# Kernel tuning notes

Hardware: AMD Instinct MI355X
Metric: run time of the kernel (lower is better)

The kernel has to match this reference:

```python
import jax, jax.numpy as jnp
import numpy as np

B, DIM, RANK, H, W = 16, 64, 32, 128, 128
E, K, BINS, FREQ_DIM, KS = 4, 2, 8, 64, 7
NOISE_STD = 1.0 / E


def dwconv(x, w, b, pad):
    # depthwise conv, NCHW, weight [C,1,kh,kw]
    y = jax.lax.conv_general_dilated(x, w, (1, 1), [(pad, pad), (pad, pad)],
        dimension_numbers=('NCHW', 'OIHW', 'NCHW'), feature_group_count=x.shape[1])
    return y + b[None, :, None, None]


def avgpool3(x):
    # AvgPool2d(3, stride=1, padding=1), count_include_pad=True -> sum/9
    s = jax.lax.reduce_window(x, 0.0, jax.lax.add, (1, 1, 3, 3), (1, 1, 1, 1),
        [(0, 0), (0, 0), (1, 1), (1, 1)])
    return s / 9.0


def freq_filter(x, gain, decay, cmax):
    # HighFreqGlobal / LowFreqGlobal: rfft2 -> scale magnitude by radial filter -> irfft2
    Bh, C, Hh, Wh = x.shape
    xf = jnp.fft.rfft2(x, norm='ortho')
    mag, ph = jnp.abs(xf), jnp.angle(xf)
    fy = jnp.fft.fftfreq(Hh).astype(x.dtype)[:, None]
    fx = jnp.fft.rfftfreq(Wh).astype(x.dtype)[None, :]
    fg = jnp.sqrt(fy ** 2 + fx ** 2)
    filt = jnp.clip((1.0 - jnp.exp(-gain * fg)) * jnp.exp(-decay * fg), 0.0, cmax)
    return jnp.fft.irfft2((mag * filt) * jnp.exp(1j * ph), s=(Hh, Wh), norm='ortho')


def freq_energy(x):
    # RoutingFunction.get_frequency_energy: radial energy histogram over BINS bins
    Bh, C, Hh, Wh = x.shape
    mag = jnp.abs(jnp.fft.fft2(x, norm='forward'))
    gy = jnp.arange(-Hh // 2, Hh // 2, dtype=jnp.float32)[:, None]
    gx = jnp.arange(-Wh // 2, Wh // 2, dtype=jnp.float32)[None, :]
    dist = jnp.sqrt(gy ** 2 + gx ** 2)
    edges = jnp.linspace(0.0, dist.max(), BINS + 1)
    masks = ((dist[None] >= edges[:-1, None, None]) & (dist[None] < edges[1:, None, None])).astype(mag.dtype)
    return jnp.einsum('bchw,khw->bk', mag, masks) / C  # sum over HW then mean over C


def setup_inputs():
    key = jax.random.key(0)
    ks = jax.random.split(key, 16)
    p = lambda k, shp, s=0.02: jax.random.normal(k, shp, jnp.float32) * s
    return {
        'x': jax.random.normal(ks[0], (B, DIM, H, W), jnp.float32),
        'noise': jax.random.normal(ks[1], (B, E), jnp.float32),
        'gate_w': p(ks[2], (E, DIM)),
        'fg_w1': p(ks[3], (FREQ_DIM, BINS)),
        'fg_b1': jnp.zeros((FREQ_DIM,), jnp.float32),
        'fg_w2': p(ks[4], (E, FREQ_DIM)),
        'proj0': p(ks[5], (E, RANK, DIM)),
        'proj1': p(ks[6], (E, RANK, DIM)),
        'proj2': p(ks[7], (E, DIM, RANK)),
        'hg_gain': jnp.float32(2.0),
        'hg_decay': jnp.float32(0.5),
        'hf_w1': p(ks[8], (RANK, 1, 3, 3), 0.1),
        'hf_b1': jnp.zeros((RANK,), jnp.float32),
        'hf_w2': p(ks[9], (RANK, 1, 3, 3), 0.1),
        'hf_b2': jnp.zeros((RANK,), jnp.float32),
        'lg_gain': jnp.float32(1.0),
        'lg_decay': jnp.float32(1.0),
        'lf_w': p(ks[10], (RANK, 1, KS, KS), 0.1),
        'lf_b': jnp.zeros((RANK,), jnp.float32),
    }


def reference(x, noise, gate_w, fg_w1, fg_b1, fg_w2, proj0, proj1, proj2,
              hg_gain, hg_decay, hf_w1, hf_b1, hf_w2, hf_b2,
              lg_gain, lg_decay, lf_w, lf_b):
    Bh = x.shape[0]
    # routing: image gate (GAP + linear) + frequency gate (MLP on radial energy)
    img_logits = jnp.mean(x, axis=(2, 3)) @ gate_w.T
    femb = freq_energy(x)
    hidden = jax.nn.relu(femb @ fg_w1.T + fg_b1)
    logits = img_logits + hidden @ fg_w2.T
    scores = jax.nn.softmax(logits + noise * NOISE_STD, axis=-1)
    vals, idx = jax.lax.top_k(scores, K)
    gates = jnp.zeros_like(scores).at[jnp.arange(Bh)[:, None], idx].set(vals)

    def expert(e, body):
        # ModExpert.process: low-rank proj -> body * silu(gate proj of shared=x) -> up proj + shortcut
        h = jnp.einsum('bchw,rc->brhw', x, proj0[e])
        g = jax.nn.silu(jnp.einsum('bchw,rc->brhw', x, proj1[e]))
        h = body(h) * g
        return jnp.einsum('brhw,cr->bchw', h, proj2[e]) + x

    gelu = lambda z: jax.nn.gelu(z, approximate=False)
    bodies = [
        lambda z: freq_filter(z, hg_gain, hg_decay, 3.0),                          # HighFreqGlobal
        lambda z: dwconv(gelu(dwconv(z, hf_w1, hf_b1, 1)), hf_w2, hf_b2, 1),       # HighFreqLocal
        lambda z: freq_filter(z, lg_gain, lg_decay, 1.0),                          # LowFreqGlobal
        lambda z: avgpool3(gelu(dwconv(z, lf_w, lf_b, KS // 2))),                  # LowFreqLocal
    ]
    # dispatch/combine expressed densely: gates are exactly zero for non-selected experts,
    # so weighted sum == SparseDispatcher.combine
    out = jnp.zeros_like(x)
    for e, body in enumerate(bodies):
        out = out + gates[:, e][:, None, None, None] * expert(e, body)
    return out
```

## Files before the change

### kernel.cpp

```cpp
#include <hip/hip_runtime.h>
#include <math.h>


namespace {

struct cpx { float x, y; };
struct TwB {
  cpx t0;
  cpx ws[6];
  float sg[6];
};

using bf16x8 = __attribute__((ext_vector_type(8))) short;
using f32x4  = __attribute__((ext_vector_type(4))) float;

__device__ __forceinline__ short f2bf(float f){
  unsigned u = __float_as_uint(f);
  u += 0x7FFF + ((u >> 16) & 1);
  return (short)(u >> 16);
}

__device__ __forceinline__ cpx cmul(cpx a, cpx b){ return {a.x*b.x - a.y*b.y, a.x*b.y + a.y*b.x}; }

__device__ __forceinline__ void init_twb(TwB &T, int lane, const float2* __restrict__ tw128){
  float2 v0 = tw128[lane];
  T.t0 = {v0.x, v0.y};
  int m = 32;
  #pragma unroll
  for (int s = 0; s < 6; s++){
    bool up = (lane & m) != 0;
    float2 wv = tw128[(lane & (m-1)) * (64/m)];
    T.ws[s] = up ? cpx{wv.x, wv.y} : cpx{1.0f, 0.0f};
    T.sg[s] = up ? -1.0f : 1.0f;
    m >>= 1;
  }
}

__device__ __forceinline__ int br6(int l){ return (int)(__brev((unsigned)l) >> 26); }
__device__ __forceinline__ int pos7(int j){ return ((j & 1) << 6) | (j >> 1); }

__device__ __forceinline__ void fft128(cpx &a, cpx &b, int lane, const TwB &T){
  cpx u{a.x + b.x, a.y + b.y};
  cpx v{a.x - b.x, a.y - b.y};
  v = cmul(v, T.t0);
  a = u; b = v;
  int m = 32;
  #pragma unroll
  for (int s = 0; s < 6; s++){
    float pax = __shfl_xor(a.x, m);
    float pay = __shfl_xor(a.y, m);
    float pbx = __shfl_xor(b.x, m);
    float pby = __shfl_xor(b.y, m);
    float sg = T.sg[s];
    cpx w = T.ws[s];
    cpx ta{fmaf(sg, a.x, pax), fmaf(sg, a.y, pay)};
    cpx tb{fmaf(sg, b.x, pbx), fmaf(sg, b.y, pby)};
    a = cmul(ta, w);
    b = cmul(tb, w);
    m >>= 1;
  }
}

__device__ __forceinline__ float gelu_exact(float v){
  return 0.5f * v * (1.0f + erff(v * 0.70710678118654752f));
}

__device__ __forceinline__ float silu(float v){
  return v / (1.0f + expf(-v));
}


__global__ __launch_bounds__(256) void k_transW(const float* __restrict__ proj0, float* __restrict__ p0t,
                                                float2* __restrict__ tw128){
  int t = threadIdx.x;
  if (t < 128){
    float s, c;
    sincosf(-6.283185307179586f * (float)t * (1.0f/128.0f), &s, &c);
    tw128[t] = make_float2(c, s);
  }
  for (int idx = t; idx < 2048; idx += 256){
    int r = idx >> 6, c = idx & 63;
    p0t[0*2048 + c*32 + r] = proj0[0*2048 + idx];
    p0t[1*2048 + c*32 + r] = proj0[2*2048 + idx];
  }
}

__global__ __launch_bounds__(512) void k_fft2fwd(const float* __restrict__ x, float2* __restrict__ X,
                                                 float* __restrict__ part_w, float* __restrict__ xmean,
                                                 const float2* __restrict__ tw128){
  __shared__ float2 z[8192];
  int bc = blockIdx.x; int t = threadIdx.x;
  int lane = t & 63, wv = t >> 6;
  TwB T; init_twb(T, lane, tw128);
  const float* img = x + (size_t)bc * 16384;
  int rb = br6(lane);

  #pragma unroll 4
  for (int k = 0; k < 8; k++){
    int p = wv*8 + k;
    int h0 = 2*p, h1 = 2*p + 1;
    cpx a{img[h0*128 + lane],      img[h1*128 + lane]};
    cpx b{img[h0*128 + lane + 64], img[h1*128 + lane + 64]};
    fft128(a, b, lane, T);
    int ia = (p << 7) | (rb ^ p);
    z[ia]      = make_float2(a.x, a.y);
    z[ia | 64] = make_float2(b.x, b.y);
  }
  __syncthreads();

  float rax[8], ray[8], rbx[8], rby[8];
  #pragma unroll
  for (int k = 0; k < 8; k++){
    int jj = wv*8 + k;
    int p  = lane >> 1, s = lane & 1;
    int p2 = 32 + p;
    cpx a, b;
    if (jj == 0){
      float2 z0  = z[(p << 7)  | (0  ^ p)];
      float2 z64 = z[(p << 7)  | (32 ^ p)];
      float2 w0  = z[(p2 << 7) | (0  ^ p2)];
      float2 w64 = z[(p2 << 7) | (32 ^ p2)];
      a = { s ? z0.y : z0.x, s ? z64.y : z64.x };
      b = { s ? w0.y : w0.x, s ? w64.y : w64.x };
    } else {
      int jm = 128 - jj;
      int pj = pos7(jj), pm = pos7(jm);
      float2 z1 = z[(p << 7) | (pj ^ p)],  z2 = z[(p << 7) | (pm ^ p)];
      if (s == 0) a = { 0.5f*(z1.x + z2.x), 0.5f*(z1.y - z2.y) };
      else        a = { 0.5f*(z1.y + z2.y), 0.5f*(z2.x - z1.x) };
      float2 w1 = z[(p2 << 7) | (pj ^ p2)], w2 = z[(p2 << 7) | (pm ^ p2)];
      if (s == 0) b = { 0.5f*(w1.x + w2.x), 0.5f*(w1.y - w2.y) };
      else        b = { 0.5f*(w1.y + w2.y), 0.5f*(w2.x - w1.x) };
    }
    fft128(a, b, lane, T);
    rax[k] = a.x; ray[k] = a.y; rbx[k] = b.x; rby[k] = b.y;
  }
  __syncthreads();
  #pragma unroll
  for (int k = 0; k < 8; k++){
    int jj = wv*8 + k;
    int ia = (jj << 7) | (rb ^ jj);
    z[ia]      = make_float2(rax[k], ray[k]);
    z[ia | 64] = make_float2(rbx[k], rby[k]);
  }
  __syncthreads();

  if (t == 0) xmean[bc] = z[0].x * (1.0f/16384.0f);

  float edges[9];
  float step = sqrtf(8192.0f) * 0.125f;
  #pragma unroll
  for (int k = 0; k <= 8; k++) edges[k] = step * (float)k;
  float acc[8] = {0,0,0,0,0,0,0,0};
  for (int idx = t; idx < 64*128; idx += 512){
    int j = idx >> 7, i = idx & 127;
    if (j == 0){
      float2 c0 = z[pos7(i)];
      int in_ = (128 - i) & 127;
      float2 d0v = z[pos7(in_)];
      float x0r = 0.5f*(c0.x + d0v.x), x0i = 0.5f*(c0.y - d0v.y);
      float x6r = 0.5f*(c0.y + d0v.y), x6i = 0.5f*(d0v.x - c0.x);
      float m0 = sqrtf(x0r*x0r + x0i*x0i) * (1.0f/16384.0f);
      float m6 = sqrtf(x6r*x6r + x6i*x6i) * (1.0f/16384.0f);
      float dyv = (float)(i - 64);
      float d0 = sqrtf(dyv*dyv + 4096.0f);
      float d6 = fabsf(dyv);
      #pragma unroll
      for (int k = 0; k < 8; k++){
        if (d0 >= edges[k] && d0 < edges[k+1]) acc[k] += m0;
        if (d6 >= edges[k] && d6 < edges[k+1]) acc[k] += m6;
      }
    } else {
      float2 zv = z[(j << 7) | (pos7(i) ^ j)];
      float mag = sqrtf(zv.x*zv.x + zv.y*zv.y) * (2.0f/16384.0f);
      float dy = (float)(i - 64), dx = (float)(j - 64);
      float d = sqrtf(dy*dy + dx*dx);
      #pragma unroll
      for (int k = 0; k < 8; k++)
        if (d >= edges[k] && d < edges[k+1]) acc[k] += mag;
    }
  }
  #pragma unroll
  for (int k = 0; k < 8; k++){
    float v = acc[k];
    for (int off = 32; off > 0; off >>= 1) v += __shfl_xor(v, off);
    if (lane == 0) part_w[(bc*8 + wv)*8 + k] = v;
  }

  float2* Xo = X + (size_t)bc * (65*128);
  for (int idx = t; idx < 65*128; idx += 512){
    int j = idx >> 7, i = idx & 127;
    float2 v;
    if (j == 0){
      float2 c0 = z[pos7(i)];
      int in_ = (128 - i) & 127;
      float2 d0v = z[pos7(in_)];
      v = make_float2(0.5f*(c0.x + d0v.x), 0.5f*(c0.y - d0v.y));
    } else if (j == 64){
      float2 c0 = z[pos7(i)];
      int in_ = (128 - i) & 127;
      float2 d0v = z[pos7(in_)];
      v = make_float2(0.5f*(c0.y + d0v.y), 0.5f*(d0v.x - c0.x));
    } else {
      v = z[(j << 7) | (pos7(i) ^ j)];
    }
    Xo[idx] = v;
  }
}

__global__ __launch_bounds__(128) void k_routing(const float* __restrict__ xmean, const float* __restrict__ part_w,
    const float* __restrict__ noise, const float* __restrict__ gate_w,
    const float* __restrict__ fg_w1, const float* __restrict__ fg_b1, const float* __restrict__ fg_w2,
    int* __restrict__ slot_e, int* __restrict__ slot_of, float* __restrict__ slot_g){
  __shared__ float femb[16][8];
  __shared__ float hid[16][64];
  __shared__ float lgt[16][4];
  int t = threadIdx.x;
  {
    int b = t >> 3, k = t & 7;
    float s = 0.f;
    for (int c = 0; c < 64; c++)
      for (int w = 0; w < 8; w++)
        s += part_w[((b*64 + c)*8 + w)*8 + k];
    femb[b][k] = s * (1.0f/64.0f);
  }
  __syncthreads();
  for (int idx = t; idx < 16*64; idx += 128){
    int b = idx >> 6, f = idx & 63;
    float s = fg_b1[f];
    for (int k = 0; k < 8; k++) s += femb[b][k] * fg_w1[f*8 + k];
    hid[b][f] = fmaxf(s, 0.f);
  }
  __syncthreads();
  if (t < 64){
    int b = t >> 2, e = t & 3;
    float s = 0.f;
    for (int c = 0; c < 64; c++) s += xmean[b*64 + c] * gate_w[e*64 + c];
    for (int f = 0; f < 64; f++) s += hid[b][f] * fg_w2[e*64 + f];
    lgt[b][e] = s + noise[b*4 + e] * 0.25f;
  }
  __syncthreads();
  if (t < 16){
    int b = t;
    float m = fmaxf(fmaxf(lgt[b][0], lgt[b][1]), fmaxf(lgt[b][2], lgt[b][3]));
    float p[4]; float sum = 0.f;
    for (int e = 0; e < 4; e++){ p[e] = expf(lgt[b][e] - m); sum += p[e]; }
    for (int e = 0; e < 4; e++) p[e] /= sum;
    int i1 = 0;
    for (int e = 1; e < 4; e++) if (p[e] > p[i1]) i1 = e;
    int i2 = -1;
    for (int e = 0; e < 4; e++){ if (e == i1) continue; if (i2 < 0 || p[e] > p[i2]) i2 = e; }
    slot_e[b*2 + 0] = i1;
    slot_e[b*2 + 1] = i2;
    slot_g[b*2 + 0] = p[i1];
    slot_g[b*2 + 1] = p[i2];
    for (int e = 0; e < 4; e++) slot_of[b*4 + e] = (e == i1) ? 0 : ((e == i2) ? 1 : -1);
  }
}

__global__ __launch_bounds__(256) void k_projfreq(const float2* __restrict__ X, const float* __restrict__ p0t,
    float2* __restrict__ Y, const int* __restrict__ slot_e,
    const float* __restrict__ hg_gain, const float* __restrict__ hg_decay,
    const float* __restrict__ lg_gain, const float* __restrict__ lg_decay){
  int b = blockIdx.z;
  int e0 = __builtin_amdgcn_readfirstlane(slot_e[b*2 + 0]);
  int e1 = __builtin_amdgcn_readfirstlane(slot_e[b*2 + 1]);
  bool f0 = (e0 == 0) || (e0 == 2);
  bool f1 = (e1 == 0) || (e1 == 2);
  if (!f0 && !f1) return;
  int j = blockIdx.y;
  int i0 = blockIdx.x * 64;
  int t = threadIdx.x;
  int lane = t & 63;
  int w = __builtin_amdgcn_readfirstlane(t >> 6);
  __shared__ float2 sx[64][64];
  for (int idx = t; idx < 4096; idx += 256){
    int c = idx >> 6, ii = idx & 63;
    sx[c][ii] = X[(((size_t)(b*64 + c))*65 + j)*128 + i0 + ii];
  }
  __syncthreads();
  int i = i0 + lane;
  const float* W0 = p0t + ((f0 ? (e0 >> 1) : (e1 >> 1)) * 2048) + w*8;
  const float* W1 = p0t + ((f1 ? (e1 >> 1) : (e0 >> 1)) * 2048) + w*8;
  float a0x[8] = {0,0,0,0,0,0,0,0}, a0y[8] = {0,0,0,0,0,0,0,0};
  float a1x[8] = {0,0,0,0,0,0,0,0}, a1y[8] = {0,0,0,0,0,0,0,0};
  for (int c = 0; c < 64; c++){
    float2 xv = sx[c][lane];
    const float* wc0 = W0 + c*32;
    const float* wc1 = W1 + c*32;
    #pragma unroll
    for (int k = 0; k < 8; k++){
      float w0v = wc0[k];
      a0x[k] += w0v * xv.x; a0y[k] += w0v * xv.y;
      float w1v = wc1[k];
      a1x[k] += w1v * xv.x; a1y[k] += w1v * xv.y;
    }
  }
  float fy = (float)(i < 64 ? i : i - 128) * (1.0f/128.0f);
  float fx = (float)j * (1.0f/128.0f);
  float fg = sqrtf(fy*fy + fx*fx);
  if (f0){
    float gain, decay, cmax;
    if (e0 == 0){ gain = *hg_gain; decay = *hg_decay; cmax = 3.0f; }
    else        { gain = *lg_gain; decay = *lg_decay; cmax = 1.0f; }
    float filt = (1.0f - expf(-gain*fg)) * expf(-decay*fg);
    filt = fminf(fmaxf(filt, 0.0f), cmax) * (1.0f/16384.0f);
    int bs = b*2 + 0;
    #pragma unroll
    for (int k = 0; k < 8; k++){
      int r = w*8 + k;
      Y[((size_t)(bs*32 + r))*8320 + j*128 + i] = make_float2(a0x[k]*filt, a0y[k]*filt);
    }
  }
  if (f1){
    float gain, decay, cmax;
    if (e1 == 0){ gain = *hg_gain; decay = *hg_decay; cmax = 3.0f; }
    else        { gain = *lg_gain; decay = *lg_decay; cmax = 1.0f; }
    float filt = (1.0f - expf(-gain*fg)) * expf(-decay*fg);
    filt = fminf(fmaxf(filt, 0.0f), cmax) * (1.0f/16384.0f);
    int bs = b*2 + 1;
    #pragma unroll
    for (int k = 0; k < 8; k++){
      int r = w*8 + k;
      Y[((size_t)(bs*32 + r))*8320 + j*128 + i] = make_float2(a1x[k]*filt, a1y[k]*filt);
    }
  }
}

__global__ __launch_bounds__(512) void k_ifft2(float2* __restrict__ Y, const int* __restrict__ slot_e,
                                               const float2* __restrict__ tw128){
  int blk = blockIdx.x;
  int bs = blk >> 5, r = blk & 31;
  int es = slot_e[bs];
  if (es == 1 || es == 3) return;
  __shared__ float2 z[8192];
  int t = threadIdx.x; int lane = t & 63, wv = t >> 6;
  TwB T; init_twb(T, lane, tw128);
  int rb = br6(lane);
  float2* Yb = Y + (size_t)(bs*32 + r) * 8320;

  for (int idx = t; idx < 8192; idx += 512){
    int j = idx >> 7, i = idx & 127;
    if (j == 0){
      float2 y0 = Yb[i];
      float2 y6 = Yb[8192 + i];
      z[pos7(i)] = make_float2(y0.x - y6.y, y0.y + y6.x);
    } else {
      z[(j << 7) | (pos7(i) ^ j)] = Yb[idx];
    }
  }
  __syncthreads();

  #pragma unroll
  for (int k = 0; k < 8; k++){
    int jj = wv*8 + k;
    float2 z0 = z[(jj << 7) | (pos7(lane) ^ jj)];
    float2 z1 = z[(jj << 7) | ((pos7(lane) + 32) ^ jj)];
    cpx a{z0.x, -z0.y}, b{z1.x, -z1.y};
    fft128(a, b, lane, T);
    int ia = (jj << 7) | (rb ^ jj);
    z[ia]      = make_float2(a.x, -a.y);
    z[ia | 64] = make_float2(b.x, -b.y);
  }
  __syncthreads();

  float* body = (float*)Yb;
  #pragma unroll 2
  for (int k = 0; k < 8; k++){
    int p = wv*8 + k;
    int h = 2*p, h1 = 2*p + 1;
    int ph = pos7(h), ph1 = pos7(h1);
    cpx a, b;
    if (lane == 0){
      float2 c0 = z[ph], c1 = z[ph1];
      a = { c0.x, c1.x };
      b = { c0.y, c1.y };
    } else {
      float2 yh = z[(lane << 7) | (ph ^ lane)];
      float2 y1 = z[(lane << 7) | (ph1 ^ lane)];
      a = { yh.x - y1.y, yh.y + y1.x };
      int lm = 64 - lane;
      float2 zh  = z[(lm << 7) | (ph ^ lm)];
      float2 z1_ = z[(lm << 7) | (ph1 ^ lm)];
      b = { zh.x + z1_.y, z1_.x - zh.y };
    }
    a.y = -a.y; b.y = -b.y;
    fft128(a, b, lane, T);
    int n0 = 2*rb;
    body[h*128 + n0]      = a.x;
    body[h1*128 + n0]     = -a.y;
    body[h*128 + n0 + 1]  = b.x;
    body[h1*128 + n0 + 1] = -b.y;
  }
}

__global__ __launch_bounds__(256) void k_projA(const float* __restrict__ x, const float* __restrict__ proj0,
    const int* __restrict__ slot_e, float* __restrict__ A){
  int b = blockIdx.y;
  int e0 = __builtin_amdgcn_readfirstlane(slot_e[b*2 + 0]);
  int e1 = __builtin_amdgcn_readfirstlane(slot_e[b*2 + 1]);
  bool c0 = (e0 == 1) || (e0 == 3);
  bool c1 = (e1 == 1) || (e1 == 3);
  if (!c0 && !c1) return;
  __shared__ unsigned short xs[128][72];
  int px0 = blockIdx.x * 128;
  int t = threadIdx.x;
  int w = t >> 6, lane = t & 63;
  int h = lane & 15, g = lane >> 4;
  const float* xb = x + (size_t)b*64*16384;

  for (int idx = t; idx < 2048; idx += 256){
    int c = idx >> 5, pq = idx & 31;
    float4 v = *(const float4*)&xb[(size_t)c*16384 + px0 + pq*4];
    xs[pq*4 + 0][c] = (unsigned short)f2bf(v.x);
    xs[pq*4 + 1][c] = (unsigned short)f2bf(v.y);
    xs[pq*4 + 2][c] = (unsigned short)f2bf(v.z);
    xs[pq*4 + 3][c] = (unsigned short)f2bf(v.w);
  }

  bf16x8 af[2][2][2];
  #pragma unroll
  for (int s = 0; s < 2; s++){
    bool cv = (s == 0) ? c0 : c1;
    if (!cv) continue;
    int e = (s == 0) ? e0 : e1;
    const float* P0 = proj0 + e*2048;
    #pragma unroll
    for (int mr = 0; mr < 2; mr++)
      #pragma unroll
      for (int k0 = 0; k0 < 2; k0++){
        const float* p = P0 + (mr*16 + h)*64 + k0*32 + g*8;
        bf16x8 v;
        #pragma unroll
        for (int j = 0; j < 8; j++) v[j] = f2bf(p[j]);
        af[s][mr][k0] = v;
      }
  }
  __syncthreads();

  int pxw = w*32;
  #pragma unroll
  for (int nt = 0; nt < 2; nt++){
    int pxl = pxw + nt*16;
    int px  = px0 + pxl;
    bf16x8 bx[2];
    #pragma unroll
    for (int k0 = 0; k0 < 2; k0++)
      bx[k0] = *(bf16x8*)&xs[pxl + h][k0*32 + g*8];
    #pragma unroll
    for (int s = 0; s < 2; s++){
      bool cv = (s == 0) ? c0 : c1;
      if (!cv) continue;
      float* Ab = A + (size_t)((b*2 + s)*32)*16384;
      #pragma unroll
      for (int mr = 0; mr < 2; mr++){
        f32x4 acc = {0.f, 0.f, 0.f, 0.f};
        acc = __builtin_amdgcn_mfma_f32_16x16x32_bf16(af[s][mr][0], bx[0], acc, 0, 0, 0);
        acc = __builtin_amdgcn_mfma_f32_16x16x32_bf16(af[s][mr][1], bx[1], acc, 0, 0, 0);
        #pragma unroll
        for (int reg = 0; reg < 4; reg++){
          int r = mr*16 + g*4 + reg;
          Ab[(size_t)r*16384 + px + h] = acc[reg];
        }
      }
    }
  }
}

__global__ __launch_bounds__(256) void k_conv3(const float* __restrict__ A, float* __restrict__ bodyY,
    const float* __restrict__ w1g, const float* __restrict__ b1g,
    const float* __restrict__ w2g, const float* __restrict__ b2g,
    const int* __restrict__ slot_of){
  int by = blockIdx.y; int b = by >> 5, r = by & 31;
  int slot = slot_of[b*4 + 1];
  if (slot < 0) return;
  int bs = b*2 + slot;
  int h0 = blockIdx.x * 16;
  int t = threadIdx.x;
  __shared__ float sin_[20*130];
  __shared__ float st[18*130];
  for (int i = t; i < 20*130; i += 256) sin_[i] = 0.f;
  for (int i = t; i < 18*130; i += 256) st[i] = 0.f;
  float w1[9], w2[9];
  #pragma unroll
  for (int k = 0; k < 9; k++){ w1[k] = w1g[r*9 + k]; w2[k] = w2g[r*9 + k]; }
  float b1 = b1g[r], b2 = b2g[r];
  __syncthreads();
  const float* ip = A + (size_t)(bs*32 + r)*16384;
  for (int idx = t; idx < 20*128; idx += 256){
    int li = idx >> 7, ww = idx & 127;
    int ih = h0 - 2 + li;
    if (ih >= 0 && ih < 128) sin_[li*130 + 1 + ww] = ip[ih*128 + ww];
  }
  __syncthreads();
  for (int idx = t; idx < 18*128; idx += 256){
    int li = idx >> 7, ww = idx & 127;
    int hs = h0 - 1 + li;
    if (hs >= 0 && hs < 128){
      float acc = b1;
      #pragma unroll
      for (int kh = 0; kh < 3; kh++)
        #pragma unroll
        for (int kw = 0; kw < 3; kw++)
          acc += w1[kh*3 + kw] * sin_[(li + kh)*130 + ww + kw];
      st[li*130 + 1 + ww] = gelu_exact(acc);
    }
  }
  __syncthreads();
  float* op = bodyY + (size_t)(bs*32 + r)*16640;
  for (int idx = t; idx < 16*128; idx += 256){
    int li = idx >> 7, ww = idx & 127;
    int ho = h0 + li;
    float acc = b2;
    #pragma unroll
    for (int kh = 0; kh < 3; kh++)
      #pragma unroll
      for (int kw = 0; kw < 3; kw++)
        acc += w2[kh*3 + kw] * st[(li + kh)*130 + ww + kw];
    op[ho*128 + ww] = acc;
  }
}

__global__ __launch_bounds__(256) void k_conv7(const float* __restrict__ A, float* __restrict__ bodyY,
    const float* __restrict__ wg, const float* __restrict__ bg,
    const int* __restrict__ slot_of){
  int by = blockIdx.y; int b = by >> 5, r = by & 31;
  int slot = slot_of[b*4 + 3];
  if (slot < 0) return;
  int bs = b*2 + slot;
  int h0 = blockIdx.x * 16;
  int t = threadIdx.x;
  __shared__ float sin_[24*134];
  __shared__ float st[18*134];
  __shared__ float wsh[49];
  for (int i = t; i < 24*134; i += 256) sin_[i] = 0.f;
  for (int i = t; i < 18*134; i += 256) st[i] = 0.f;
  if (t < 49) wsh[t] = wg[r*49 + t];
  float bias = bg[r];
  __syncthreads();
  const float* ip = A + (size_t)(bs*32 + r)*16384;
  for (int idx = t; idx < 24*128; idx += 256){
    int li = idx >> 7, ww = idx & 127;
    int ih = h0 - 4 + li;
    if (ih >= 0 && ih < 128) sin_[li*134 + 3 + ww] = ip[ih*128 + ww];
  }
  __syncthreads();
  for (int idx = t; idx < 18*128; idx += 256){
    int li = idx >> 7, ww = idx & 127;
    int hs = h0 - 1 + li;
    if (hs >= 0 && hs < 128){
      float acc = bias;
      #pragma unroll
      for (int kh = 0; kh < 7; kh++)
        #pragma unroll
        for (int kw = 0; kw < 7; kw++)
          acc += wsh[kh*7 + kw] * sin_[(li + kh)*134 + ww + kw];
      st[li*134 + 1 + ww] = gelu_exact(acc);
    }
  }
  __syncthreads();
  float* op = bodyY + (size_t)(bs*32 + r)*16640;
  for (int idx = t; idx < 16*128; idx += 256){
    int li = idx >> 7, ww = idx & 127;
    int ho = h0 + li;
    float acc = 0.f;
    #pragma unroll
    for (int kh = 0; kh < 3; kh++)
      #pragma unroll
      for (int kw = 0; kw < 3; kw++)
        acc += st[(li + kh)*134 + ww + kw];
    op[ho*128 + ww] = acc * (1.0f/9.0f);
  }
}

__global__ __launch_bounds__(256) void k_combine(const float* __restrict__ x, const float* __restrict__ bodyY,
    const float* __restrict__ proj1, const float* __restrict__ proj2,
    const int* __restrict__ slot_e, const float* __restrict__ slot_g,
    float* __restrict__ out){
  __shared__ __align__(16) unsigned char smem[57344];
  unsigned short (*xs)[72]            = (unsigned short(*)[72])(smem);
  unsigned short (*bs2)[128][36]      = (unsigned short(*)[128][36])(smem + 18432);
  unsigned short (*sblk)[4][2][16][40] = (unsigned short(*)[4][2][16][40])(smem + 36864);
  float* obuf = (float*)smem;

  int b = blockIdx.y;
  int px0 = blockIdx.x * 128;
  int t = threadIdx.x;
  int w = t >> 6, lane = t & 63;
  int h = lane & 15, g = lane >> 4;
  int ea = __builtin_amdgcn_readfirstlane(slot_e[b*2 + 0]);
  int eb = __builtin_amdgcn_readfirstlane(slot_e[b*2 + 1]);
  float ga = slot_g[b*2 + 0], gb = slot_g[b*2 + 1];
  float gs = ga + gb;

  const float* xb = x + (size_t)b*64*16384;
  float* ob = out + (size_t)b*64*16384;
  const float* Bd0 = bodyY + (size_t)(b*2 + 0)*32*16640;
  const float* Bd1 = bodyY + (size_t)(b*2 + 1)*32*16640;

  for (int idx = t; idx < 2048; idx += 256){
    int c = idx >> 5, pq = idx & 31;
    float4 v = *(const float4*)&xb[(size_t)c*16384 + px0 + pq*4];
    xs[pq*4 + 0][c] = (unsigned short)f2bf(v.x);
    xs[pq*4 + 1][c] = (unsigned short)f2bf(v.y);
    xs[pq*4 + 2][c] = (unsigned short)f2bf(v.z);
    xs[pq*4 + 3][c] = (unsigned short)f2bf(v.w);
  }
  for (int idx = t; idx < 2048; idx += 256){
    int s = idx >> 10, r = (idx >> 5) & 31, pq = idx & 31;
    const float* Bod = (s == 0) ? Bd0 : Bd1;
    float4 v = *(const float4*)&Bod[(size_t)r*16640 + px0 + pq*4];
    bs2[s][pq*4 + 0][r] = (unsigned short)f2bf(v.x);
    bs2[s][pq*4 + 1][r] = (unsigned short)f2bf(v.y);
    bs2[s][pq*4 + 2][r] = (unsigned short)f2bf(v.z);
    bs2[s][pq*4 + 3][r] = (unsigned short)f2bf(v.w);
  }

  bf16x8 a1[2][2][2];
  #pragma unroll
  for (int s = 0; s < 2; s++){
    const float* P1 = proj1 + (s == 0 ? ea : eb)*2048;
    #pragma unroll
    for (int mr = 0; mr < 2; mr++)
      #pragma unroll
      for (int k0 = 0; k0 < 2; k0++){
        const float* p = P1 + (mr*16 + h)*64 + k0*32 + g*8;
        bf16x8 v;
        #pragma unroll
        for (int j = 0; j < 8; j++) v[j] = f2bf(p[j]);
        a1[s][mr][k0] = v;
      }
  }
  bf16x8 a2[2][4];
  #pragma unroll
  for (int s = 0; s < 2; s++){
    const float* P2 = proj2 + (s == 0 ? ea : eb)*2048;
    #pragma unroll
    for (int mc = 0; mc < 4; mc++){
      const float* p = P2 + (mc*16 + h)*32 + g*8;
      bf16x8 v;
      #pragma unroll
      for (int j = 0; j < 8; j++) v[j] = f2bf(p[j]);
      a2[s][mc] = v;
    }
  }
  __syncthreads();

  int pxw = w*32;
  #pragma unroll
  for (int nt = 0; nt < 2; nt++){
    int pxl = pxw + nt*16;
    bf16x8 bx[2];
    #pragma unroll
    for (int k0 = 0; k0 < 2; k0++)
      bx[k0] = *(bf16x8*)&xs[pxl + h][k0*32 + g*8];
    f32x4 acc1[2][2];
    #pragma unroll
    for (int s = 0; s < 2; s++)
      #pragma unroll
      for (int mr = 0; mr < 2; mr++){
        f32x4 acc = {0.f, 0.f, 0.f, 0.f};
        acc = __builtin_amdgcn_mfma_f32_16x16x32_bf16(a1[s][mr][0], bx[0], acc, 0, 0, 0);
        acc = __builtin_amdgcn_mfma_f32_16x16x32_bf16(a1[s][mr][1], bx[1], acc, 0, 0, 0);
        acc1[s][mr] = acc;
      }
    #pragma unroll
    for (int s = 0; s < 2; s++){
      float gw = (s == 0) ? ga : gb;
      #pragma unroll
      for (int mr = 0; mr < 2; mr++){
        int r0 = mr*16 + g*4;
        unsigned short b4[4];
        *(uint2*)b4 = *(uint2*)&bs2[s][pxl + h][r0];
        unsigned pk0, pk1;
        {
          float bv0 = __uint_as_float(((unsigned)b4[0]) << 16);
          float bv1 = __uint_as_float(((unsigned)b4[1]) << 16);
          float bv2 = __uint_as_float(((unsigned)b4[2]) << 16);
          float bv3 = __uint_as_float(((unsigned)b4[3]) << 16);
          float s0 = gw * bv0 * silu(acc1[s][mr][0]);
          float s1 = gw * bv1 * silu(acc1[s][mr][1]);
          float s2 = gw * bv2 * silu(acc1[s][mr][2]);
          float s3 = gw * bv3 * silu(acc1[s][mr][3]);
          pk0 = (unsigned)(unsigned short)f2bf(s0) | ((unsigned)(unsigned short)f2bf(s1) << 16);
          pk1 = (unsigned)(unsigned short)f2bf(s2) | ((unsigned)(unsigned short)f2bf(s3) << 16);
        }
        uint2 pv; pv.x = pk0; pv.y = pk1;
        *(uint2*)&sblk[nt][w][s][h][r0] = pv;
      }
    }
  }
  __syncthreads();

  #pragma unroll
  for (int nt = 0; nt < 2; nt++){
    bf16x8 sb0 = *(bf16x8*)&sblk[nt][w][0][h][g*8];
    bf16x8 sb1 = *(bf16x8*)&sblk[nt][w][1][h][g*8];
    #pragma unroll
    for (int mc = 0; mc < 4; mc++){
      f32x4 acc = {0.f, 0.f, 0.f, 0.f};
      acc = __builtin_amdgcn_mfma_f32_16x16x32_bf16(a2[0][mc], sb0, acc, 0, 0, 0);
      acc = __builtin_amdgcn_mfma_f32_16x16x32_bf16(a2[1][mc], sb1, acc, 0, 0, 0);
      #pragma unroll
      for (int reg = 0; reg < 4; reg++){
        int c = mc*16 + g*4 + reg;
        obuf[(w*64 + c)*36 + nt*16 + h] = acc[reg];
      }
    }
  }
  int fq = lane & 7, cr = lane >> 3;
  const float* xw = xb + px0 + w*32;
  float* ow = ob + px0 + w*32;
  #pragma unroll
  for (int i = 0; i < 8; i++){
    int c = i*8 + cr;
    float4 v = *(float4*)&obuf[(w*64 + c)*36 + fq*4];
    float4 xv4 = *(const float4*)&xw[(size_t)c*16384 + fq*4];
    *(float4*)&ow[(size_t)c*16384 + fq*4] =
      make_float4(gs*xv4.x + v.x, gs*xv4.y + v.y, gs*xv4.z + v.z, gs*xv4.w + v.w);
  }
}

}

extern "C" void kernel_launch(void* const* d_in, const int* in_sizes, int n_in,
                              void* d_out, int out_size, void* d_ws, size_t ws_size,
                              hipStream_t stream) {
  (void)in_sizes; (void)n_in; (void)out_size; (void)ws_size;
  const float* x        = (const float*)d_in[0];
  const float* noise    = (const float*)d_in[1];
  const float* gate_w   = (const float*)d_in[2];
  const float* fg_w1    = (const float*)d_in[3];
  const float* fg_b1    = (const float*)d_in[4];
  const float* fg_w2    = (const float*)d_in[5];
  const float* proj0    = (const float*)d_in[6];
  const float* proj1    = (const float*)d_in[7];
  const float* proj2    = (const float*)d_in[8];
  const float* hg_gain  = (const float*)d_in[9];
  const float* hg_decay = (const float*)d_in[10];
  const float* hf_w1    = (const float*)d_in[11];
  const float* hf_b1    = (const float*)d_in[12];
  const float* hf_w2    = (const float*)d_in[13];
  const float* hf_b2    = (const float*)d_in[14];
  const float* lg_gain  = (const float*)d_in[15];
  const float* lg_decay = (const float*)d_in[16];
  const float* lf_w     = (const float*)d_in[17];
  const float* lf_b     = (const float*)d_in[18];
  float* out = (float*)d_out;

  float* ws = (float*)d_ws;
  float2* X  = (float2*)ws;
  float*  A  = ws;
  float*  Yf = ws + 17039360;
  float2* Y2 = (float2*)Yf;
  float*  tail   = ws + 34078720;
  float*  xmean  = tail;
  float*  part_w = xmean + 1024;
  float*  p0t    = part_w + 65536;
  float*  tw128f = p0t + 4096;
  float2* tw128  = (float2*)tw128f;
  float*  slot_g = tw128f + 256;
  int*    slot_e = (int*)(slot_g + 32);
  int*    slot_of = slot_e + 32;

  k_transW<<<1, 256, 0, stream>>>(proj0, p0t, tw128);
  k_fft2fwd<<<1024, 512, 0, stream>>>(x, X, part_w, xmean, tw128);
  k_routing<<<1, 128, 0, stream>>>(xmean, part_w, noise, gate_w, fg_w1, fg_b1, fg_w2,
                                   slot_e, slot_of, slot_g);

  k_projfreq<<<dim3(2,65,16), 256, 0, stream>>>(X, p0t, Y2, slot_e,
                                                hg_gain, hg_decay, lg_gain, lg_decay);

  k_projA<<<dim3(128,16), 256, 0, stream>>>(x, proj0, slot_e, A);

  k_ifft2<<<1024, 512, 0, stream>>>(Y2, slot_e, tw128);

  k_conv3<<<dim3(8,512), 256, 0, stream>>>(A, Yf, hf_w1, hf_b1, hf_w2, hf_b2, slot_of);
  k_conv7<<<dim3(8,512), 256, 0, stream>>>(A, Yf, lf_w, lf_b, slot_of);

  k_combine<<<dim3(128,16), 256, 0, stream>>>(x, Yf, proj1, proj2, slot_e, slot_g, out);
}
```

Measured before the change: 306.3 us.

## Merge small kernels to cut launches and compute twiddles in-kernel

```diff
diff --git a/kernel.cpp b/kernel.cpp
--- a/kernel.cpp
+++ b/kernel.cpp
@@ -70,28 +70,19 @@
 }
 
 
-__global__ __launch_bounds__(256) void k_transW(const float* __restrict__ proj0, float* __restrict__ p0t,
-                                                float2* __restrict__ tw128){
-  int t = threadIdx.x;
+__global__ __launch_bounds__(512) void k_fft2fwd(const float* __restrict__ x, float2* __restrict__ X,
+                                                 float* __restrict__ part_w, float* __restrict__ xmean){
+  __shared__ float2 z[8192];
+  int bc = blockIdx.x; int t = threadIdx.x;
+  int lane = t & 63, wv = t >> 6;
   if (t < 128){
     float s, c;
     sincosf(-6.283185307179586f * (float)t * (1.0f/128.0f), &s, &c);
-    tw128[t] = make_float2(c, s);
-  }
-  for (int idx = t; idx < 2048; idx += 256){
-    int r = idx >> 6, c = idx & 63;
-    p0t[0*2048 + c*32 + r] = proj0[0*2048 + idx];
-    p0t[1*2048 + c*32 + r] = proj0[2*2048 + idx];
-  }
-}
-
-__global__ __launch_bounds__(512) void k_fft2fwd(const float* __restrict__ x, float2* __restrict__ X,
-                                                 float* __restrict__ part_w, float* __restrict__ xmean,
-                                                 const float2* __restrict__ tw128){
-  __shared__ float2 z[8192];
-  int bc = blockIdx.x; int t = threadIdx.x;
-  int lane = t & 63, wv = t >> 6;
-  TwB T; init_twb(T, lane, tw128);
+    z[t] = make_float2(c, s);
+  }
+  __syncthreads();
+  TwB T; init_twb(T, lane, (const float2*)z);
+  __syncthreads();
   const float* img = x + (size_t)bc * 16384;
   int rb = br6(lane);
 
@@ -211,11 +202,17 @@
 __global__ __launch_bounds__(128) void k_routing(const float* __restrict__ xmean, const float* __restrict__ part_w,
     const float* __restrict__ noise, const float* __restrict__ gate_w,
     const float* __restrict__ fg_w1, const float* __restrict__ fg_b1, const float* __restrict__ fg_w2,
+    const float* __restrict__ proj0, float* __restrict__ p0t,
     int* __restrict__ slot_e, int* __restrict__ slot_of, float* __restrict__ slot_g){
   __shared__ float femb[16][8];
   __shared__ float hid[16][64];
   __shared__ float lgt[16][4];
   int t = threadIdx.x;
+  for (int idx = t; idx < 2048; idx += 128){
+    int r = idx >> 6, c = idx & 63;
+    p0t[0*2048 + c*32 + r] = proj0[0*2048 + idx];
+    p0t[1*2048 + c*32 + r] = proj0[2*2048 + idx];
+  }
   {
     int b = t >> 3, k = t & 7;
     float s = 0.f;
@@ -327,249 +324,254 @@
   }
 }
 
-__global__ __launch_bounds__(512) void k_ifft2(float2* __restrict__ Y, const int* __restrict__ slot_e,
-                                               const float2* __restrict__ tw128){
-  int blk = blockIdx.x;
-  int bs = blk >> 5, r = blk & 31;
-  int es = slot_e[bs];
-  if (es == 1 || es == 3) return;
-  __shared__ float2 z[8192];
-  int t = threadIdx.x; int lane = t & 63, wv = t >> 6;
-  TwB T; init_twb(T, lane, tw128);
-  int rb = br6(lane);
-  float2* Yb = Y + (size_t)(bs*32 + r) * 8320;
-
-  for (int idx = t; idx < 8192; idx += 512){
-    int j = idx >> 7, i = idx & 127;
-    if (j == 0){
-      float2 y0 = Yb[i];
-      float2 y6 = Yb[8192 + i];
-      z[pos7(i)] = make_float2(y0.x - y6.y, y0.y + y6.x);
-    } else {
-      z[(j << 7) | (pos7(i) ^ j)] = Yb[idx];
-    }
-  }
-  __syncthreads();
-
-  #pragma unroll
-  for (int k = 0; k < 8; k++){
-    int jj = wv*8 + k;
-    float2 z0 = z[(jj << 7) | (pos7(lane) ^ jj)];
-    float2 z1 = z[(jj << 7) | ((pos7(lane) + 32) ^ jj)];
-    cpx a{z0.x, -z0.y}, b{z1.x, -z1.y};
-    fft128(a, b, lane, T);
-    int ia = (jj << 7) | (rb ^ jj);
-    z[ia]      = make_float2(a.x, -a.y);
-    z[ia | 64] = make_float2(b.x, -b.y);
-  }
-  __syncthreads();
-
-  float* body = (float*)Yb;
-  #pragma unroll 2
-  for (int k = 0; k < 8; k++){
-    int p = wv*8 + k;
-    int h = 2*p, h1 = 2*p + 1;
-    int ph = pos7(h), ph1 = pos7(h1);
-    cpx a, b;
-    if (lane == 0){
-      float2 c0 = z[ph], c1 = z[ph1];
-      a = { c0.x, c1.x };
-      b = { c0.y, c1.y };
-    } else {
-      float2 yh = z[(lane << 7) | (ph ^ lane)];
-      float2 y1 = z[(lane << 7) | (ph1 ^ lane)];
-      a = { yh.x - y1.y, yh.y + y1.x };
-      int lm = 64 - lane;
-      float2 zh  = z[(lm << 7) | (ph ^ lm)];
-      float2 z1_ = z[(lm << 7) | (ph1 ^ lm)];
-      b = { zh.x + z1_.y, z1_.x - zh.y };
-    }
-    a.y = -a.y; b.y = -b.y;
-    fft128(a, b, lane, T);
-    int n0 = 2*rb;
-    body[h*128 + n0]      = a.x;
-    body[h1*128 + n0]     = -a.y;
-    body[h*128 + n0 + 1]  = b.x;
-    body[h1*128 + n0 + 1] = -b.y;
-  }
-}
-
-__global__ __launch_bounds__(256) void k_projA(const float* __restrict__ x, const float* __restrict__ proj0,
-    const int* __restrict__ slot_e, float* __restrict__ A){
-  int b = blockIdx.y;
-  int e0 = __builtin_amdgcn_readfirstlane(slot_e[b*2 + 0]);
-  int e1 = __builtin_amdgcn_readfirstlane(slot_e[b*2 + 1]);
-  bool c0 = (e0 == 1) || (e0 == 3);
-  bool c1 = (e1 == 1) || (e1 == 3);
-  if (!c0 && !c1) return;
-  __shared__ unsigned short xs[128][72];
-  int px0 = blockIdx.x * 128;
+__global__ __launch_bounds__(512) void k_ifta(float2* __restrict__ Y, const int* __restrict__ slot_e,
+    const float* __restrict__ x, const float* __restrict__ proj0, float* __restrict__ A){
+  __shared__ __align__(16) unsigned char ubuf[65536];
+  int bid = blockIdx.x;
   int t = threadIdx.x;
-  int w = t >> 6, lane = t & 63;
-  int h = lane & 15, g = lane >> 4;
-  const float* xb = x + (size_t)b*64*16384;
-
-  for (int idx = t; idx < 2048; idx += 256){
-    int c = idx >> 5, pq = idx & 31;
-    float4 v = *(const float4*)&xb[(size_t)c*16384 + px0 + pq*4];
-    xs[pq*4 + 0][c] = (unsigned short)f2bf(v.x);
-    xs[pq*4 + 1][c] = (unsigned short)f2bf(v.y);
-    xs[pq*4 + 2][c] = (unsigned short)f2bf(v.z);
-    xs[pq*4 + 3][c] = (unsigned short)f2bf(v.w);
-  }
-
-  bf16x8 af[2][2][2];
-  #pragma unroll
-  for (int s = 0; s < 2; s++){
-    bool cv = (s == 0) ? c0 : c1;
-    if (!cv) continue;
-    int e = (s == 0) ? e0 : e1;
-    const float* P0 = proj0 + e*2048;
-    #pragma unroll
-    for (int mr = 0; mr < 2; mr++)
-      #pragma unroll
-      for (int k0 = 0; k0 < 2; k0++){
-        const float* p = P0 + (mr*16 + h)*64 + k0*32 + g*8;
-        bf16x8 v;
-        #pragma unroll
-        for (int j = 0; j < 8; j++) v[j] = f2bf(p[j]);
-        af[s][mr][k0] = v;
-      }
-  }
-  __syncthreads();
-
-  int pxw = w*32;
-  #pragma unroll
-  for (int nt = 0; nt < 2; nt++){
-    int pxl = pxw + nt*16;
-    int px  = px0 + pxl;
-    bf16x8 bx[2];
-    #pragma unroll
-    for (int k0 = 0; k0 < 2; k0++)
-      bx[k0] = *(bf16x8*)&xs[pxl + h][k0*32 + g*8];
+  if (bid < 1024){
+    int bs = bid >> 5, r = bid & 31;
+    int es = slot_e[bs];
+    if (es == 1 || es == 3) return;
+    float2* z = (float2*)ubuf;
+    int lane = t & 63, wv = t >> 6;
+    if (t < 128){
+      float s, c;
+      sincosf(-6.283185307179586f * (float)t * (1.0f/128.0f), &s, &c);
+      z[t] = make_float2(c, s);
+    }
+    __syncthreads();
+    TwB T; init_twb(T, lane, (const float2*)z);
+    __syncthreads();
+    int rb = br6(lane);
+    float2* Yb = Y + (size_t)(bs*32 + r) * 8320;
+
+    for (int idx = t; idx < 8192; idx += 512){
+      int j = idx >> 7, i = idx & 127;
+      if (j == 0){
+        float2 y0 = Yb[i];
+        float2 y6 = Yb[8192 + i];
+        z[pos7(i)] = make_float2(y0.x - y6.y, y0.y + y6.x);
+      } else {
+        z[(j << 7) | (pos7(i) ^ j)] = Yb[idx];
+      }
+    }
+    __syncthreads();
+
+    #pragma unroll
+    for (int k = 0; k < 8; k++){
+      int jj = wv*8 + k;
+      float2 z0 = z[(jj << 7) | (pos7(lane) ^ jj)];
+      float2 z1 = z[(jj << 7) | ((pos7(lane) + 32) ^ jj)];
+      cpx a{z0.x, -z0.y}, b{z1.x, -z1.y};
+      fft128(a, b, lane, T);
+      int ia = (jj << 7) | (rb ^ jj);
+      z[ia]      = make_float2(a.x, -a.y);
+      z[ia | 64] = make_float2(b.x, -b.y);
+    }
+    __syncthreads();
+
+    float* body = (float*)Yb;
+    #pragma unroll 2
+    for (int k = 0; k < 8; k++){
+      int p = wv*8 + k;
+      int h = 2*p, h1 = 2*p + 1;
+      int ph = pos7(h), ph1 = pos7(h1);
+      cpx a, b;
+      if (lane == 0){
+        float2 c0 = z[ph], c1 = z[ph1];
+        a = { c0.x, c1.x };
+        b = { c0.y, c1.y };
+      } else {
+        float2 yh = z[(lane << 7) | (ph ^ lane)];
+        float2 y1 = z[(lane << 7) | (ph1 ^ lane)];
+        a = { yh.x - y1.y, yh.y + y1.x };
+        int lm = 64 - lane;
+        float2 zh  = z[(lm << 7) | (ph ^ lm)];
+        float2 z1_ = z[(lm << 7) | (ph1 ^ lm)];
+        b = { zh.x + z1_.y, z1_.x - zh.y };
+      }
+      a.y = -a.y; b.y = -b.y;
+      fft128(a, b, lane, T);
+      int n0 = 2*rb;
+      body[h*128 + n0]      = a.x;
+      body[h1*128 + n0]     = -a.y;
+      body[h*128 + n0 + 1]  = b.x;
+      body[h1*128 + n0 + 1] = -b.y;
+    }
+  } else {
+    int aid = bid - 1024;
+    int b = aid >> 6;
+    int e0 = __builtin_amdgcn_readfirstlane(slot_e[b*2 + 0]);
+    int e1 = __builtin_amdgcn_readfirstlane(slot_e[b*2 + 1]);
+    bool c0 = (e0 == 1) || (e0 == 3);
+    bool c1 = (e1 == 1) || (e1 == 3);
+    if (!c0 && !c1) return;
+    unsigned short (*xs)[72] = (unsigned short(*)[72])ubuf;
+    int px0 = (aid & 63) * 256;
+    int w = t >> 6, lane = t & 63;
+    int h = lane & 15, g = lane >> 4;
+    const float* xb = x + (size_t)b*64*16384;
+
+    for (int idx = t; idx < 4096; idx += 512){
+      int c = idx >> 6, pq = idx & 63;
+      float4 v = *(const float4*)&xb[(size_t)c*16384 + px0 + pq*4];
+      xs[pq*4 + 0][c] = (unsigned short)f2bf(v.x);
+      xs[pq*4 + 1][c] = (unsigned short)f2bf(v.y);
+      xs[pq*4 + 2][c] = (unsigned short)f2bf(v.z);
+      xs[pq*4 + 3][c] = (unsigned short)f2bf(v.w);
+    }
+
+    bf16x8 af[2][2][2];
     #pragma unroll
     for (int s = 0; s < 2; s++){
       bool cv = (s == 0) ? c0 : c1;
       if (!cv) continue;
-      float* Ab = A + (size_t)((b*2 + s)*32)*16384;
-      #pragma unroll
-      for (int mr = 0; mr < 2; mr++){
-        f32x4 acc = {0.f, 0.f, 0.f, 0.f};
-        acc = __builtin_amdgcn_mfma_f32_16x16x32_bf16(af[s][mr][0], bx[0], acc, 0, 0, 0);
-        acc = __builtin_amdgcn_mfma_f32_16x16x32_bf16(af[s][mr][1], bx[1], acc, 0, 0, 0);
+      int e = (s == 0) ? e0 : e1;
+      const float* P0 = proj0 + e*2048;
+      #pragma unroll
+      for (int mr = 0; mr < 2; mr++)
         #pragma unroll
-        for (int reg = 0; reg < 4; reg++){
-          int r = mr*16 + g*4 + reg;
-          Ab[(size_t)r*16384 + px + h] = acc[reg];
+        for (int k0 = 0; k0 < 2; k0++){
+          const float* p = P0 + (mr*16 + h)*64 + k0*32 + g*8;
+          bf16x8 v;
+          #pragma unroll
+          for (int j = 0; j < 8; j++) v[j] = f2bf(p[j]);
+          af[s][mr][k0] = v;
         }
-      }
-    }
-  }
-}
-
-__global__ __launch_bounds__(256) void k_conv3(const float* __restrict__ A, float* __restrict__ bodyY,
+    }
+    __syncthreads();
+
+    int pxw = w*32;
+    #pragma unroll
+    for (int nt = 0; nt < 2; nt++){
+      int pxl = pxw + nt*16;
+      int px  = px0 + pxl;
+      bf16x8 bx[2];
+      #pragma unroll
+      for (int k0 = 0; k0 < 2; k0++)
+        bx[k0] = *(bf16x8*)&xs[pxl + h][k0*32 + g*8];
+      #pragma unroll
+      for (int s = 0; s < 2; s++){
+        bool cv = (s == 0) ? c0 : c1;
+        if (!cv) continue;
+        float* Ab = A + (size_t)((b*2 + s)*32)*16384;
+        #pragma unroll
+        for (int mr = 0; mr < 2; mr++){
+          f32x4 acc = {0.f, 0.f, 0.f, 0.f};
+          acc = __builtin_amdgcn_mfma_f32_16x16x32_bf16(af[s][mr][0], bx[0], acc, 0, 0, 0);
+          acc = __builtin_amdgcn_mfma_f32_16x16x32_bf16(af[s][mr][1], bx[1], acc, 0, 0, 0);
+          #pragma unroll
+          for (int reg = 0; reg < 4; reg++){
+            int r = mr*16 + g*4 + reg;
+            Ab[(size_t)r*16384 + px + h] = acc[reg];
+          }
+        }
+      }
+    }
+  }
+}
+
+__global__ __launch_bounds__(256) void k_conv(const float* __restrict__ A, float* __restrict__ bodyY,
     const float* __restrict__ w1g, const float* __restrict__ b1g,
     const float* __restrict__ w2g, const float* __restrict__ b2g,
+    const float* __restrict__ wg, const float* __restrict__ bg,
     const int* __restrict__ slot_of){
+  __shared__ __align__(16) float cbuf[5680];
   int by = blockIdx.y; int b = by >> 5, r = by & 31;
-  int slot = slot_of[b*4 + 1];
-  if (slot < 0) return;
-  int bs = b*2 + slot;
   int h0 = blockIdx.x * 16;
   int t = threadIdx.x;
-  __shared__ float sin_[20*130];
-  __shared__ float st[18*130];
-  for (int i = t; i < 20*130; i += 256) sin_[i] = 0.f;
-  for (int i = t; i < 18*130; i += 256) st[i] = 0.f;
-  float w1[9], w2[9];
-  #pragma unroll
-  for (int k = 0; k < 9; k++){ w1[k] = w1g[r*9 + k]; w2[k] = w2g[r*9 + k]; }
-  float b1 = b1g[r], b2 = b2g[r];
-  __syncthreads();
-  const float* ip = A + (size_t)(bs*32 + r)*16384;
-  for (int idx = t; idx < 20*128; idx += 256){
-    int li = idx >> 7, ww = idx & 127;
-    int ih = h0 - 2 + li;
-    if (ih >= 0 && ih < 128) sin_[li*130 + 1 + ww] = ip[ih*128 + ww];
-  }
-  __syncthreads();
-  for (int idx = t; idx < 18*128; idx += 256){
-    int li = idx >> 7, ww = idx & 127;
-    int hs = h0 - 1 + li;
-    if (hs >= 0 && hs < 128){
-      float acc = b1;
+  if (blockIdx.z == 0){
+    int slot = slot_of[b*4 + 1];
+    if (slot < 0) return;
+    int bs = b*2 + slot;
+    float* sin_ = cbuf;
+    float* st   = cbuf + 2600;
+    for (int i = t; i < 20*130; i += 256) sin_[i] = 0.f;
+    for (int i = t; i < 18*130; i += 256) st[i] = 0.f;
+    float w1[9], w2[9];
+    #pragma unroll
+    for (int k = 0; k < 9; k++){ w1[k] = w1g[r*9 + k]; w2[k] = w2g[r*9 + k]; }
+    float b1 = b1g[r], b2 = b2g[r];
+    __syncthreads();
+    const float* ip = A + (size_t)(bs*32 + r)*16384;
+    for (int idx = t; idx < 20*128; idx += 256){
+      int li = idx >> 7, ww = idx & 127;
+      int ih = h0 - 2 + li;
+      if (ih >= 0 && ih < 128) sin_[li*130 + 1 + ww] = ip[ih*128 + ww];
+    }
+    __syncthreads();
+    for (int idx = t; idx < 18*128; idx += 256){
+      int li = idx >> 7, ww = idx & 127;
+      int hs = h0 - 1 + li;
+      if (hs >= 0 && hs < 128){
+        float acc = b1;
+        #pragma unroll
+        for (int kh = 0; kh < 3; kh++)
+          #pragma unroll
+          for (int kw = 0; kw < 3; kw++)
+            acc += w1[kh*3 + kw] * sin_[(li + kh)*130 + ww + kw];
+        st[li*130 + 1 + ww] = gelu_exact(acc);
+      }
+    }
+    __syncthreads();
+    float* op = bodyY + (size_t)(bs*32 + r)*16640;
+    for (int idx = t; idx < 16*128; idx += 256){
+      int li = idx >> 7, ww = idx & 127;
+      int ho = h0 + li;
+      float acc = b2;
       #pragma unroll
       for (int kh = 0; kh < 3; kh++)
         #pragma unroll
         for (int kw = 0; kw < 3; kw++)
-          acc += w1[kh*3 + kw] * sin_[(li + kh)*130 + ww + kw];
-      st[li*130 + 1 + ww] = gelu_exact(acc);
-    }
-  }
-  __syncthreads();
-  float* op = bodyY + (size_t)(bs*32 + r)*16640;
-  for (int idx = t; idx < 16*128; idx += 256){
-    int li = idx >> 7, ww = idx & 127;
-    int ho = h0 + li;
-    float acc = b2;
-    #pragma unroll
-    for (int kh = 0; kh < 3; kh++)
-      #pragma unroll
-      for (int kw = 0; kw < 3; kw++)
-        acc += w2[kh*3 + kw] * st[(li + kh)*130 + ww + kw];
-    op[ho*128 + ww] = acc;
-  }
-}
-
-__global__ __launch_bounds__(256) void k_conv7(const float* __restrict__ A, float* __restrict__ bodyY,
-    const float* __restrict__ wg, const float* __restrict__ bg,
-    const int* __restrict__ slot_of){
-  int by = blockIdx.y; int b = by >> 5, r = by & 31;
-  int slot = slot_of[b*4 + 3];
-  if (slot < 0) return;
-  int bs = b*2 + slot;
-  int h0 = blockIdx.x * 16;
-  int t = threadIdx.x;
-  __shared__ float sin_[24*134];
-  __shared__ float st[18*134];
-  __shared__ float wsh[49];
-  for (int i = t; i < 24*134; i += 256) sin_[i] = 0.f;
-  for (int i = t; i < 18*134; i += 256) st[i] = 0.f;
-  if (t < 49) wsh[t] = wg[r*49 + t];
-  float bias = bg[r];
-  __syncthreads();
-  const float* ip = A + (size_t)(bs*32 + r)*16384;
-  for (int idx = t; idx < 24*128; idx += 256){
-    int li = idx >> 7, ww = idx & 127;
-    int ih = h0 - 4 + li;
-    if (ih >= 0 && ih < 128) sin_[li*134 + 3 + ww] = ip[ih*128 + ww];
-  }
-  __syncthreads();
-  for (int idx = t; idx < 18*128; idx += 256){
-    int li = idx >> 7, ww = idx & 127;
-    int hs = h0 - 1 + li;
-    if (hs >= 0 && hs < 128){
-      float acc = bias;
-      #pragma unroll
-      for (int kh = 0; kh < 7; kh++)
+          acc += w2[kh*3 + kw] * st[(li + kh)*130 + ww + kw];
+      op[ho*128 + ww] = acc;
+    }
+  } else {
+    int slot = slot_of[b*4 + 3];
+    if (slot < 0) return;
+    int bs = b*2 + slot;
+    float* sin_ = cbuf;
+    float* st   = cbuf + 3216;
+    float* wsh  = cbuf + 5628;
+    for (int i = t; i < 24*134; i += 256) sin_[i] = 0.f;
+    for (int i = t; i < 18*134; i += 256) st[i] = 0.f;
+    if (t < 49) wsh[t] = wg[r*49 + t];
+    float bias = bg[r];
+    __syncthreads();
+    const float* ip = A + (size_t)(bs*32 + r)*16384;
+    for (int idx = t; idx < 24*128; idx += 256){
+      int li = idx >> 7, ww = idx & 127;
+      int ih = h0 - 4 + li;
+      if (ih >= 0 && ih < 128) sin_[li*134 + 3 + ww] = ip[ih*128 + ww];
+    }
+    __syncthreads();
+    for (int idx = t; idx < 18*128; idx += 256){
+      int li = idx >> 7, ww = idx & 127;
+      int hs = h0 - 1 + li;
+      if (hs >= 0 && hs < 128){
+        float acc = bias;
         #pragma unroll
-        for (int kw = 0; kw < 7; kw++)
-          acc += wsh[kh*7 + kw] * sin_[(li + kh)*134 + ww + kw];
-      st[li*134 + 1 + ww] = gelu_exact(acc);
-    }
-  }
-  __syncthreads();
-  float* op = bodyY + (size_t)(bs*32 + r)*16640;
-  for (int idx = t; idx < 16*128; idx += 256){
-    int li = idx >> 7, ww = idx & 127;
-    int ho = h0 + li;
-    float acc = 0.f;
-    #pragma unroll
-    for (int kh = 0; kh < 3; kh++)
-      #pragma unroll
-      for (int kw = 0; kw < 3; kw++)
-        acc += st[(li + kh)*134 + ww + kw];
-    op[ho*128 + ww] = acc * (1.0f/9.0f);
+        for (int kh = 0; kh < 7; kh++)
+          #pragma unroll
+          for (int kw = 0; kw < 7; kw++)
+            acc += wsh[kh*7 + kw] * sin_[(li + kh)*134 + ww + kw];
+        st[li*134 + 1 + ww] = gelu_exact(acc);
+      }
+    }
+    __syncthreads();
+    float* op = bodyY + (size_t)(bs*32 + r)*16640;
+    for (int idx = t; idx < 16*128; idx += 256){
+      int li = idx >> 7, ww = idx & 127;
+      int ho = h0 + li;
+      float acc = 0.f;
+      #pragma unroll
+      for (int kh = 0; kh < 3; kh++)
+        #pragma unroll
+        for (int kw = 0; kw < 3; kw++)
+          acc += st[(li + kh)*134 + ww + kw];
+      op[ho*128 + ww] = acc * (1.0f/9.0f);
+    }
   }
 }
 
@@ -757,26 +759,17 @@
   float*  xmean  = tail;
   float*  part_w = xmean + 1024;
   float*  p0t    = part_w + 65536;
-  float*  tw128f = p0t + 4096;
-  float2* tw128  = (float2*)tw128f;
-  float*  slot_g = tw128f + 256;
+  float*  slot_g = p0t + 4096;
   int*    slot_e = (int*)(slot_g + 32);
   int*    slot_of = slot_e + 32;
 
-  k_transW<<<1, 256, 0, stream>>>(proj0, p0t, tw128);
-  k_fft2fwd<<<1024, 512, 0, stream>>>(x, X, part_w, xmean, tw128);
+  k_fft2fwd<<<1024, 512, 0, stream>>>(x, X, part_w, xmean);
   k_routing<<<1, 128, 0, stream>>>(xmean, part_w, noise, gate_w, fg_w1, fg_b1, fg_w2,
-                                   slot_e, slot_of, slot_g);
-
+                                   proj0, p0t, slot_e, slot_of, slot_g);
   k_projfreq<<<dim3(2,65,16), 256, 0, stream>>>(X, p0t, Y2, slot_e,
                                                 hg_gain, hg_decay, lg_gain, lg_decay);
-
-  k_projA<<<dim3(128,16), 256, 0, stream>>>(x, proj0, slot_e, A);
-
-  k_ifft2<<<1024, 512, 0, stream>>>(Y2, slot_e, tw128);
-
-  k_conv3<<<dim3(8,512), 256, 0, stream>>>(A, Yf, hf_w1, hf_b1, hf_w2, hf_b2, slot_of);
-  k_conv7<<<dim3(8,512), 256, 0, stream>>>(A, Yf, lf_w, lf_b, slot_of);
-
+  k_ifta<<<2048, 512, 0, stream>>>(Y2, slot_e, x, proj0, A);
+  k_conv<<<dim3(8,512,2), 256, 0, stream>>>(A, Yf, hf_w1, hf_b1, hf_w2, hf_b2,
+                                            lf_w, lf_b, slot_of);
   k_combine<<<dim3(128,16), 256, 0, stream>>>(x, Yf, proj1, proj2, slot_e, slot_g, out);
 }
```

Result: faster. 299.3 us (median of 2 runs) (-2.3%).
